# Optimization experiments

Measured on AMD Instinct MI355X. Metric: run time of the kernel, lower is better.

## Reference

```python
import jax, jax.numpy as jnp
import numpy as np

FS = 3          # filter_size
B, C, H, W = 16, 256, 96, 96
BN_EPS = 1e-5


def setup_inputs() -> dict:
    key = jax.random.key(0)
    ks = jax.random.split(key, 6)
    s = 0.05
    return {
        "x": jax.random.normal(ks[0], (B, C, H, W), jnp.float32),
        "convoluted": jax.random.normal(ks[1], (B, C, H, W), jnp.float32),
        # filter_gen_conv: 1x1 Conv2d(C -> C)
        "w_gen": jax.random.normal(ks[2], (C, C, 1, 1), jnp.float32) * s,
        "b_gen": jax.random.normal(ks[3], (C,), jnp.float32) * s,
        # c1: 3x3 Conv2d(C -> C) + BatchNorm2d(C) + ReLU
        "w_c1": jax.random.normal(ks[4], (C, C, 3, 3), jnp.float32) * s,
        "b_c1": jax.random.normal(ks[5], (C,), jnp.float32) * s,
        "gamma": jnp.ones((C,), jnp.float32),
        "beta": jnp.zeros((C,), jnp.float32),
    }


def reference(x, convoluted, w_gen, b_gen, w_c1, b_c1, gamma, beta):
    b, c, h, w = x.shape
    # adaptive_avg_pool2d(x, FS): H,W divisible by FS -> uniform bins
    pooled = x.reshape(b, c, FS, h // FS, FS, w // FS).mean(axis=(3, 5))  # [b,c,FS,FS]
    # 1x1 conv generating per-sample per-channel filters
    gen = jnp.einsum('bcij,oc->boij', pooled, w_gen[:, :, 0, 0]) + b_gen[None, :, None, None]

    # c1: conv3x3 (pad 1) + BatchNorm (training-mode batch stats) + ReLU
    y = jax.lax.conv_general_dilated(
        convoluted, w_c1, window_strides=(1, 1), padding=((1, 1), (1, 1)),
        dimension_numbers=('NCHW', 'OIHW', 'NCHW')) + b_c1[None, :, None, None]
    mu = y.mean(axis=(0, 2, 3), keepdims=True)
    var = y.var(axis=(0, 2, 3), keepdims=True)
    y = (y - mu) * jax.lax.rsqrt(var + BN_EPS)
    y = jax.nn.relu(y * gamma[None, :, None, None] + beta[None, :, None, None])

    # dynamic per-sample depthwise conv: groups = b*c, symmetric pad (FS odd)
    y = y.reshape(1, b * c, h, w)
    filt = gen.reshape(b * c, 1, FS, FS)
    pad = (FS - 1) // 2
    out = jax.lax.conv_general_dilated(
        y, filt, window_strides=(1, 1), padding=((pad, pad), (pad, pad)),
        feature_group_count=b * c, dimension_numbers=('NCHW', 'OIHW', 'NCHW'))
    return out.reshape(b, c, h, w)
```

## Files before the change

kernel.cpp:

```cpp
#include <hip/hip_runtime.h>

typedef __bf16 bf16x8 __attribute__((ext_vector_type(8)));
typedef float f32x4 __attribute__((ext_vector_type(4)));

static __device__ __forceinline__ ushort f2b(float f) {
    uint32_t x = __float_as_uint(f);
    x += 0x7fffu + ((x >> 16) & 1u);
    return (ushort)(x >> 16);
}
static __device__ __forceinline__ float b2f(ushort u) {
    return __uint_as_float(((uint32_t)u) << 16);
}

typedef const __attribute__((address_space(1))) uint32_t gu32;
typedef __attribute__((address_space(3))) uint32_t lu32;
static __device__ __forceinline__ void gl_lds16(const void* g, void* l) {
    __builtin_amdgcn_global_load_lds((gu32*)g, (lu32*)l, 16, 0, 0);
}

__global__ __launch_bounds__(256) void pool_k(const float* __restrict__ x,
                                              float* __restrict__ pooled) {
    const int bc  = blockIdx.x;
    const int tid = threadIdx.x;
    const int lane = tid & 63, wv = tid >> 6;
    const float4* p4 = (const float4*)(x + (size_t)bc * 9216);
    __shared__ float red[4][9];
#pragma unroll
    for (int bi = 0; bi < 3; ++bi) {
#pragma unroll
        for (int bj = 0; bj < 3; ++bj) {
            int row = bi * 32 + (tid >> 3);
            int c4  = bj * 8 + (tid & 7);
            float4 f = p4[row * 24 + c4];
            float s = f.x + f.y + f.z + f.w;
#pragma unroll
            for (int off = 32; off; off >>= 1) s += __shfl_down(s, off);
            if (lane == 0) red[wv][bi * 3 + bj] = s;
        }
    }
    __syncthreads();
    if (tid < 9) {
        float s = red[0][tid] + red[1][tid] + red[2][tid] + red[3][tid];
        pooled[(size_t)bc * 9 + tid] = s * (1.0f / 1024.0f);
    }
}

__global__ __launch_bounds__(256) void gen_k(const float* __restrict__ pooled,
                                             const float* __restrict__ wgen,
                                             const float* __restrict__ bgen,
                                             float* __restrict__ gen) {
    __shared__ float pl[256];
    const int b = blockIdx.x / 9, ij = blockIdx.x % 9;
    const int o = threadIdx.x;
    pl[o] = pooled[((size_t)b * 256 + o) * 9 + ij];
    __syncthreads();
    float a = bgen[o];
    const float4* wg4 = (const float4*)(wgen + (size_t)o * 256);
    const float4* pl4 = (const float4*)pl;
#pragma unroll 4
    for (int q = 0; q < 64; ++q) {
        float4 w = wg4[q], p = pl4[q];
        a += w.x * p.x + w.y * p.y + w.z * p.z + w.w * p.w;
    }
    gen[((size_t)b * 256 + o) * 9 + ij] = a;
}

__global__ __launch_bounds__(256) void wtr_k(const float* __restrict__ wc1,
                                             ushort* __restrict__ wtr) {
    int g = blockIdx.x * 256 + threadIdx.x;
    int step = g >> 10;
    int hi   = (g >> 8) & 3;
    int row  = g & 255;
    int ch = step / 9, tap = step - ch * 9;
    int cbase = ch * 32 + hi * 8;
    ushort tmp[8];
#pragma unroll
    for (int j = 0; j < 8; ++j)
        tmp[j] = f2b(wc1[(size_t)row * 2304 + (size_t)(cbase + j) * 9 + tap]);
    *(uint4*)(wtr + (size_t)g * 8) = *(const uint4*)tmp;
}

__global__ __launch_bounds__(512) void conv_k(const float* __restrict__ xin,
                                              const ushort* __restrict__ wtr,
                                              const float* __restrict__ bc1,
                                              ushort* __restrict__ yb) {
    __shared__ ushort Al[2][8192];
    __shared__ ushort Bl[15680];

    const int blk = blockIdx.x;
    const int b = blk / 48, hg = blk % 48, h0 = hg * 2;
    const int tid = threadIdx.x;
    const int lane = tid & 63, wv = tid >> 6;
    const int wm = wv & 3, wn = wv >> 2;
    const int lo = lane & 15, hi = lane >> 4;

    if (tid < 256) {
        int row = tid >> 6, pxp = ((tid >> 5) & 1) ? 97 : 0, c = tid & 31;
        Bl[(row * 98 + pxp) * 40 + c] = 0;
    }

    const int aoff0 = wv * 1024 + lane * 8;
    const int aoff1 = aoff0 + 512;

    const float* gsrc[6];
    int loff[6];
    bool vld[6];
#pragma unroll
    for (int it = 0; it < 6; ++it) {
        int id = tid + it * 512;
        int c = id & 31, rq = id >> 5;
        int row = rq / 24, q = rq - row * 24;
        int r = h0 + row - 1;
        vld[it] = ((unsigned)r < 96u);
        int rs = vld[it] ? r : 0;
        gsrc[it] = xin + (size_t)b * 2359296 + (size_t)c * 9216 + rs * 96 + q * 4;
        loff[it] = (row * 98 + q * 4 + 1) * 40 + c;
    }

    int aro[4];
#pragma unroll
    for (int mi = 0; mi < 4; ++mi)
        aro[mi] = hi * 2048 + (wm * 64 + mi * 16 + lo) * 8;

    f32x4 acc[4][6] = {};
    float4 f[6];

    gl_lds16(wtr + aoff0, &Al[0][wv * 1024]);
    gl_lds16(wtr + aoff1, &Al[0][wv * 1024 + 512]);
#pragma unroll
    for (int it = 0; it < 6; ++it) f[it] = *(const float4*)gsrc[it];
#pragma unroll
    for (int it = 0; it < 6; ++it) {
        ushort u0 = 0, u1 = 0, u2 = 0, u3 = 0;
        if (vld[it]) { u0 = f2b(f[it].x); u1 = f2b(f[it].y);
                       u2 = f2b(f[it].z); u3 = f2b(f[it].w); }
        ushort* wp = &Bl[loff[it]];
        wp[0] = u0; wp[40] = u1; wp[80] = u2; wp[120] = u3;
    }
    __syncthreads();

    int stp = 0;
    for (int ch = 0; ch < 8; ++ch) {
        if (ch < 7) {
#pragma unroll
            for (int it = 0; it < 6; ++it)
                f[it] = *(const float4*)(gsrc[it] + (size_t)(ch + 1) * 294912);
        }
#pragma unroll
        for (int tap = 0; tap < 9; ++tap, ++stp) {
            const int buf = stp & 1;
            if (stp < 71) {
                const ushort* as = wtr + (size_t)(stp + 1) * 8192;
                gl_lds16(as + aoff0, &Al[buf ^ 1][wv * 1024]);
                gl_lds16(as + aoff1, &Al[buf ^ 1][wv * 1024 + 512]);
            }
            const int dy = tap / 3, dx = tap % 3;
            bf16x8 af[4], bfr[6];
            const ushort* Ab = &Al[buf][0];
#pragma unroll
            for (int mi = 0; mi < 4; ++mi)
                af[mi] = *(const bf16x8*)(Ab + aro[mi]);
            const ushort* Bp = &Bl[((wn + dy) * 98 + lo + dx) * 40 + hi * 8];
#pragma unroll
            for (int ni = 0; ni < 6; ++ni)
                bfr[ni] = *(const bf16x8*)(Bp + ni * 640);
#pragma unroll
            for (int mi = 0; mi < 4; ++mi)
#pragma unroll
                for (int ni = 0; ni < 6; ++ni)
                    acc[mi][ni] = __builtin_amdgcn_mfma_f32_16x16x32_bf16(
                        af[mi], bfr[ni], acc[mi][ni], 0, 0, 0);
            if (tap == 8) {
                if (ch < 7) {
                    __syncthreads();
#pragma unroll
                    for (int it = 0; it < 6; ++it) {
                        ushort u0 = 0, u1 = 0, u2 = 0, u3 = 0;
                        if (vld[it]) { u0 = f2b(f[it].x); u1 = f2b(f[it].y);
                                       u2 = f2b(f[it].z); u3 = f2b(f[it].w); }
                        ushort* wp = &Bl[loff[it]];
                        wp[0] = u0; wp[40] = u1; wp[80] = u2; wp[120] = u3;
                    }
                    __syncthreads();
                }
            } else {
                __syncthreads();
            }
        }
    }

    const size_t ybase = (size_t)b * 2359296 + (size_t)(h0 + wn) * 96;
#pragma unroll
    for (int mi = 0; mi < 4; ++mi) {
        const int o0 = wm * 64 + mi * 16 + hi * 4;
#pragma unroll
        for (int rr = 0; rr < 4; ++rr) {
            const int o = o0 + rr;
            const float bias = bc1[o];
#pragma unroll
            for (int ni = 0; ni < 6; ++ni) {
                const int px = ni * 16 + lo;
                yb[ybase + (size_t)o * 9216 + px] = f2b(acc[mi][ni][rr] + bias);
            }
        }
    }
}

__global__ __launch_bounds__(256) void bnstat_k(const ushort* __restrict__ yb,
                                                float* __restrict__ part) {
    const int bc = blockIdx.x, tid = threadIdx.x;
    const ushort4* p4 = (const ushort4*)(yb + (size_t)bc * 9216);
    float s = 0.f, s2 = 0.f;
#pragma unroll
    for (int it = 0; it < 9; ++it) {
        ushort4 u = p4[tid + it * 256];
        float a = b2f(u.x), bb = b2f(u.y), c = b2f(u.z), d = b2f(u.w);
        s  += a + bb + c + d;
        s2 += a * a + bb * bb + c * c + d * d;
    }
    const int lane = tid & 63, wv = tid >> 6;
#pragma unroll
    for (int off = 32; off; off >>= 1) {
        s += __shfl_down(s, off);
        s2 += __shfl_down(s2, off);
    }
    __shared__ float r1[4], r2[4];
    if (lane == 0) { r1[wv] = s; r2[wv] = s2; }
    __syncthreads();
    if (tid == 0) part[bc]        = r1[0] + r1[1] + r1[2] + r1[3];
    if (tid == 1) part[4096 + bc] = r2[0] + r2[1] + r2[2] + r2[3];
}

__global__ __launch_bounds__(256) void bnfin_k(const float* __restrict__ part,
                                               const float* __restrict__ gamma,
                                               const float* __restrict__ beta,
                                               float* __restrict__ bnp) {
    const int c = threadIdx.x;
    float s = 0.f, s2 = 0.f;
#pragma unroll
    for (int b = 0; b < 16; ++b) {
        s  += part[b * 256 + c];
        s2 += part[4096 + b * 256 + c];
    }
    const float invN = 1.0f / 147456.0f;
    float mu  = s * invN;
    float var = s2 * invN - mu * mu;
    float sc  = gamma[c] * rsqrtf(var + 1e-5f);
    bnp[c]       = sc;
    bnp[256 + c] = beta[c] - mu * sc;
}

__global__ __launch_bounds__(256) void dw_k(const ushort* __restrict__ yb,
                                            const float* __restrict__ gen,
                                            const float* __restrict__ bnp,
                                            float* __restrict__ out) {
    __shared__ float pl[9216];
    const int bc = blockIdx.x, tid = threadIdx.x;
    const int c = bc & 255;
    const float sc = bnp[c], sh = bnp[256 + c];
    const ushort4* p4 = (const ushort4*)(yb + (size_t)bc * 9216);
#pragma unroll
    for (int it = 0; it < 9; ++it) {
        int v = tid + it * 256;
        ushort4 u = p4[v];
        float4 f;
        f.x = fmaxf(b2f(u.x) * sc + sh, 0.f);
        f.y = fmaxf(b2f(u.y) * sc + sh, 0.f);
        f.z = fmaxf(b2f(u.z) * sc + sh, 0.f);
        f.w = fmaxf(b2f(u.w) * sc + sh, 0.f);
        *(float4*)&pl[v * 4] = f;
    }
    float g[9];
    const float* gp = gen + (size_t)bc * 9;
#pragma unroll
    for (int k = 0; k < 9; ++k) g[k] = gp[k];
    __syncthreads();
    float* op = out + (size_t)bc * 9216;
#pragma unroll
    for (int it = 0; it < 36; ++it) {
        int i = tid + it * 256;
        int row = i / 96, col = i - row * 96;
        float a = 0.f;
#pragma unroll
        for (int dy = 0; dy < 3; ++dy) {
            int rr = row + dy - 1;
            if (rr < 0 || rr >= 96) continue;
#pragma unroll
            for (int dxq = 0; dxq < 3; ++dxq) {
                int cc = col + dxq - 1;
                if (cc < 0 || cc >= 96) continue;
                a += pl[rr * 96 + cc] * g[dy * 3 + dxq];
            }
        }
        op[i] = a;
    }
}

extern "C" void kernel_launch(void* const* d_in, const int* in_sizes, int n_in,
                              void* d_out, int out_size, void* d_ws, size_t ws_size,
                              hipStream_t stream) {
    const float* x       = (const float*)d_in[0];
    const float* conv_in = (const float*)d_in[1];
    const float* w_gen   = (const float*)d_in[2];
    const float* b_gen   = (const float*)d_in[3];
    const float* w_c1    = (const float*)d_in[4];
    const float* b_c1    = (const float*)d_in[5];
    const float* gamma   = (const float*)d_in[6];
    const float* beta    = (const float*)d_in[7];
    float* out = (float*)d_out;

    char* ws = (char*)d_ws;
    float*  pooled = (float*)(ws + 0);
    float*  gen    = (float*)(ws + 147456);
    ushort* wtr    = (ushort*)(ws + 294912);
    float*  part   = (float*)(ws + 1474560);
    float*  bnp    = (float*)(ws + 1507328);
    ushort* yb     = (ushort*)(ws + 1509376);

    pool_k  <<<4096, 256, 0, stream>>>(x, pooled);
    gen_k   <<<144,  256, 0, stream>>>(pooled, w_gen, b_gen, gen);
    wtr_k   <<<288,  256, 0, stream>>>(w_c1, wtr);
    conv_k  <<<768,  512, 0, stream>>>(conv_in, wtr, b_c1, yb);
    bnstat_k<<<4096, 256, 0, stream>>>(yb, part);
    bnfin_k <<<1,    256, 0, stream>>>(part, gamma, beta, bnp);
    dw_k    <<<4096, 256, 0, stream>>>(yb, gen, bnp, out);
}
```

Baseline: 383.0 us.

## Fuse BN statistics into conv epilogue and load weights directly to registers

The conv kernel now accumulates per-channel sum and sum-of-squares in its epilogue and writes partials, so the separate bnstat pass that re-read the bf16 conv output is gone. A new per-channel reduction kernel replaces the single-block finalize. Weight tiles now go straight from global memory into registers with double buffering instead of through LDS via global_load_lds. This drops one LDS buffer and many barriers, restructuring the channel-chunk loop into pairs. The cost is more register pressure and global weight loads that are not shared across waves.

```diff
diff --git a/kernel.cpp b/kernel.cpp
--- a/kernel.cpp
+++ b/kernel.cpp
@@ -10,12 +10,6 @@
 }
 static __device__ __forceinline__ float b2f(ushort u) {
     return __uint_as_float(((uint32_t)u) << 16);
-}
-
-typedef const __attribute__((address_space(1))) uint32_t gu32;
-typedef __attribute__((address_space(3))) uint32_t lu32;
-static __device__ __forceinline__ void gl_lds16(const void* g, void* l) {
-    __builtin_amdgcn_global_load_lds((gu32*)g, (lu32*)l, 16, 0, 0);
 }
 
 __global__ __launch_bounds__(256) void pool_k(const float* __restrict__ x,
@@ -69,22 +63,22 @@
                                              ushort* __restrict__ wtr) {
     int g = blockIdx.x * 256 + threadIdx.x;
     int step = g >> 10;
-    int hi   = (g >> 8) & 3;
-    int row  = g & 255;
+    int row  = (g >> 2) & 255;
+    int c8   = g & 3;
     int ch = step / 9, tap = step - ch * 9;
-    int cbase = ch * 32 + hi * 8;
+    int cb = ch * 32 + c8 * 8;
     ushort tmp[8];
 #pragma unroll
     for (int j = 0; j < 8; ++j)
-        tmp[j] = f2b(wc1[(size_t)row * 2304 + (size_t)(cbase + j) * 9 + tap]);
+        tmp[j] = f2b(wc1[(size_t)row * 2304 + (size_t)(cb + j) * 9 + tap]);
     *(uint4*)(wtr + (size_t)g * 8) = *(const uint4*)tmp;
 }
 
 __global__ __launch_bounds__(512) void conv_k(const float* __restrict__ xin,
                                               const ushort* __restrict__ wtr,
                                               const float* __restrict__ bc1,
-                                              ushort* __restrict__ yb) {
-    __shared__ ushort Al[2][8192];
+                                              ushort* __restrict__ yb,
+                                              float* __restrict__ part) {
     __shared__ ushort Bl[15680];
 
     const int blk = blockIdx.x;
@@ -98,9 +92,6 @@
         int row = tid >> 6, pxp = ((tid >> 5) & 1) ? 97 : 0, c = tid & 31;
         Bl[(row * 98 + pxp) * 40 + c] = 0;
     }
-
-    const int aoff0 = wv * 1024 + lane * 8;
-    const int aoff1 = aoff0 + 512;
 
     const float* gsrc[6];
     int loff[6];
@@ -117,74 +108,74 @@
         loff[it] = (row * 98 + q * 4 + 1) * 40 + c;
     }
 
-    int aro[4];
-#pragma unroll
-    for (int mi = 0; mi < 4; ++mi)
-        aro[mi] = hi * 2048 + (wm * 64 + mi * 16 + lo) * 8;
+    float4 f[6];
+    auto stageB = [&]() {
+#pragma unroll
+        for (int it = 0; it < 6; ++it) {
+            ushort u0 = 0, u1 = 0, u2 = 0, u3 = 0;
+            if (vld[it]) { u0 = f2b(f[it].x); u1 = f2b(f[it].y);
+                           u2 = f2b(f[it].z); u3 = f2b(f[it].w); }
+            ushort* wp = &Bl[loff[it]];
+            wp[0] = u0; wp[40] = u1; wp[80] = u2; wp[120] = u3;
+        }
+    };
+
+    const int agrain = (wm * 64 + lo) * 4 + hi;
 
     f32x4 acc[4][6] = {};
-    float4 f[6];
-
-    gl_lds16(wtr + aoff0, &Al[0][wv * 1024]);
-    gl_lds16(wtr + aoff1, &Al[0][wv * 1024 + 512]);
+    uint4 abuf[2][4];
+
+    {
+        const uint4* Ap = (const uint4*)wtr + agrain;
+#pragma unroll
+        for (int mi = 0; mi < 4; ++mi) abuf[0][mi] = Ap[mi * 64];
+    }
 #pragma unroll
     for (int it = 0; it < 6; ++it) f[it] = *(const float4*)gsrc[it];
-#pragma unroll
-    for (int it = 0; it < 6; ++it) {
-        ushort u0 = 0, u1 = 0, u2 = 0, u3 = 0;
-        if (vld[it]) { u0 = f2b(f[it].x); u1 = f2b(f[it].y);
-                       u2 = f2b(f[it].z); u3 = f2b(f[it].w); }
-        ushort* wp = &Bl[loff[it]];
-        wp[0] = u0; wp[40] = u1; wp[80] = u2; wp[120] = u3;
-    }
-    __syncthreads();
-
-    int stp = 0;
-    for (int ch = 0; ch < 8; ++ch) {
-        if (ch < 7) {
-#pragma unroll
-            for (int it = 0; it < 6; ++it)
-                f[it] = *(const float4*)(gsrc[it] + (size_t)(ch + 1) * 294912);
-        }
-#pragma unroll
-        for (int tap = 0; tap < 9; ++tap, ++stp) {
-            const int buf = stp & 1;
-            if (stp < 71) {
-                const ushort* as = wtr + (size_t)(stp + 1) * 8192;
-                gl_lds16(as + aoff0, &Al[buf ^ 1][wv * 1024]);
-                gl_lds16(as + aoff1, &Al[buf ^ 1][wv * 1024 + 512]);
-            }
+    stageB();
+    __syncthreads();
+
+    for (int k = 0; k < 4; ++k) {
+#pragma unroll
+        for (int it = 0; it < 6; ++it)
+            f[it] = *(const float4*)(gsrc[it] + (size_t)(2 * k + 1) * 294912);
+#pragma unroll
+        for (int t = 0; t < 18; ++t) {
+            const int cur = t & 1;
+            if (t < 17 || k < 3) {
+                const uint4* Ap =
+                    (const uint4*)(wtr + (size_t)(k * 18 + t + 1) * 8192) + agrain;
+#pragma unroll
+                for (int mi = 0; mi < 4; ++mi) abuf[cur ^ 1][mi] = Ap[mi * 64];
+            }
+            const int tap = (t < 9) ? t : t - 9;
             const int dy = tap / 3, dx = tap % 3;
-            bf16x8 af[4], bfr[6];
-            const ushort* Ab = &Al[buf][0];
-#pragma unroll
-            for (int mi = 0; mi < 4; ++mi)
-                af[mi] = *(const bf16x8*)(Ab + aro[mi]);
+            bf16x8 bfr[6];
             const ushort* Bp = &Bl[((wn + dy) * 98 + lo + dx) * 40 + hi * 8];
 #pragma unroll
             for (int ni = 0; ni < 6; ++ni)
                 bfr[ni] = *(const bf16x8*)(Bp + ni * 640);
 #pragma unroll
-            for (int mi = 0; mi < 4; ++mi)
+            for (int mi = 0; mi < 4; ++mi) {
+                const bf16x8 af = *(const bf16x8*)&abuf[cur][mi];
 #pragma unroll
                 for (int ni = 0; ni < 6; ++ni)
                     acc[mi][ni] = __builtin_amdgcn_mfma_f32_16x16x32_bf16(
-                        af[mi], bfr[ni], acc[mi][ni], 0, 0, 0);
-            if (tap == 8) {
-                if (ch < 7) {
-                    __syncthreads();
-#pragma unroll
-                    for (int it = 0; it < 6; ++it) {
-                        ushort u0 = 0, u1 = 0, u2 = 0, u3 = 0;
-                        if (vld[it]) { u0 = f2b(f[it].x); u1 = f2b(f[it].y);
-                                       u2 = f2b(f[it].z); u3 = f2b(f[it].w); }
-                        ushort* wp = &Bl[loff[it]];
-                        wp[0] = u0; wp[40] = u1; wp[80] = u2; wp[120] = u3;
-                    }
-                    __syncthreads();
+                        af, bfr[ni], acc[mi][ni], 0, 0, 0);
+            }
+            if (t == 8) {
+                __syncthreads();
+                stageB();
+                __syncthreads();
+                if (k < 3) {
+#pragma unroll
+                    for (int it = 0; it < 6; ++it)
+                        f[it] = *(const float4*)(gsrc[it] + (size_t)(2 * k + 2) * 294912);
                 }
-            } else {
+            } else if (t == 17 && k < 3) {
                 __syncthreads();
+                stageB();
+                __syncthreads();
             }
         }
     }
@@ -192,62 +183,69 @@
     const size_t ybase = (size_t)b * 2359296 + (size_t)(h0 + wn) * 96;
 #pragma unroll
     for (int mi = 0; mi < 4; ++mi) {
-        const int o0 = wm * 64 + mi * 16 + hi * 4;
+        float s[4], s2[4];
 #pragma unroll
         for (int rr = 0; rr < 4; ++rr) {
-            const int o = o0 + rr;
+            const int o = wm * 64 + mi * 16 + hi * 4 + rr;
             const float bias = bc1[o];
+            float sv = 0.f, sv2 = 0.f;
 #pragma unroll
             for (int ni = 0; ni < 6; ++ni) {
                 const int px = ni * 16 + lo;
-                yb[ybase + (size_t)o * 9216 + px] = f2b(acc[mi][ni][rr] + bias);
-            }
-        }
-    }
-}
-
-__global__ __launch_bounds__(256) void bnstat_k(const ushort* __restrict__ yb,
-                                                float* __restrict__ part) {
-    const int bc = blockIdx.x, tid = threadIdx.x;
-    const ushort4* p4 = (const ushort4*)(yb + (size_t)bc * 9216);
-    float s = 0.f, s2 = 0.f;
-#pragma unroll
-    for (int it = 0; it < 9; ++it) {
-        ushort4 u = p4[tid + it * 256];
-        float a = b2f(u.x), bb = b2f(u.y), c = b2f(u.z), d = b2f(u.w);
-        s  += a + bb + c + d;
-        s2 += a * a + bb * bb + c * c + d * d;
-    }
-    const int lane = tid & 63, wv = tid >> 6;
-#pragma unroll
-    for (int off = 32; off; off >>= 1) {
-        s += __shfl_down(s, off);
-        s2 += __shfl_down(s2, off);
-    }
-    __shared__ float r1[4], r2[4];
-    if (lane == 0) { r1[wv] = s; r2[wv] = s2; }
-    __syncthreads();
-    if (tid == 0) part[bc]        = r1[0] + r1[1] + r1[2] + r1[3];
-    if (tid == 1) part[4096 + bc] = r2[0] + r2[1] + r2[2] + r2[3];
-}
-
-__global__ __launch_bounds__(256) void bnfin_k(const float* __restrict__ part,
+                float v = acc[mi][ni][rr] + bias;
+                yb[ybase + (size_t)o * 9216 + px] = f2b(v);
+                sv += v; sv2 += v * v;
+            }
+            s[rr] = sv; s2[rr] = sv2;
+        }
+#pragma unroll
+        for (int off = 1; off < 16; off <<= 1) {
+#pragma unroll
+            for (int rr = 0; rr < 4; ++rr) {
+                s[rr]  += __shfl_xor(s[rr], off);
+                s2[rr] += __shfl_xor(s2[rr], off);
+            }
+        }
+        if (lo == 0) {
+#pragma unroll
+            for (int rr = 0; rr < 4; ++rr) {
+                const int o = wm * 64 + mi * 16 + hi * 4 + rr;
+                part[(size_t)o * 1536 + blk * 2 + wn]          = s[rr];
+                part[393216 + (size_t)o * 1536 + blk * 2 + wn] = s2[rr];
+            }
+        }
+    }
+}
+
+__global__ __launch_bounds__(256) void bnred_k(const float* __restrict__ part,
                                                const float* __restrict__ gamma,
                                                const float* __restrict__ beta,
                                                float* __restrict__ bnp) {
-    const int c = threadIdx.x;
+    const int o = blockIdx.x, t = threadIdx.x;
+    const float* p0 = part + (size_t)o * 1536;
+    const float* p1 = p0 + 393216;
     float s = 0.f, s2 = 0.f;
 #pragma unroll
-    for (int b = 0; b < 16; ++b) {
-        s  += part[b * 256 + c];
-        s2 += part[4096 + b * 256 + c];
-    }
-    const float invN = 1.0f / 147456.0f;
-    float mu  = s * invN;
-    float var = s2 * invN - mu * mu;
-    float sc  = gamma[c] * rsqrtf(var + 1e-5f);
-    bnp[c]       = sc;
-    bnp[256 + c] = beta[c] - mu * sc;
+    for (int k = 0; k < 6; ++k) { s += p0[t + k * 256]; s2 += p1[t + k * 256]; }
+    const int lane = t & 63, wv = t >> 6;
+#pragma unroll
+    for (int off = 32; off; off >>= 1) {
+        s  += __shfl_down(s, off);
+        s2 += __shfl_down(s2, off);
+    }
+    __shared__ float r1[4], r2[4];
+    if (lane == 0) { r1[wv] = s; r2[wv] = s2; }
+    __syncthreads();
+    if (t == 0) {
+        float S  = r1[0] + r1[1] + r1[2] + r1[3];
+        float S2 = r2[0] + r2[1] + r2[2] + r2[3];
+        const float invN = 1.0f / 147456.0f;
+        float mu  = S * invN;
+        float var = S2 * invN - mu * mu;
+        float sc  = gamma[o] * rsqrtf(var + 1e-5f);
+        bnp[o]       = sc;
+        bnp[256 + o] = beta[o] - mu * sc;
+    }
 }
 
 __global__ __launch_bounds__(256) void dw_k(const ushort* __restrict__ yb,
@@ -314,14 +312,13 @@
     float*  gen    = (float*)(ws + 147456);
     ushort* wtr    = (ushort*)(ws + 294912);
     float*  part   = (float*)(ws + 1474560);
-    float*  bnp    = (float*)(ws + 1507328);
-    ushort* yb     = (ushort*)(ws + 1509376);
-
-    pool_k  <<<4096, 256, 0, stream>>>(x, pooled);
-    gen_k   <<<144,  256, 0, stream>>>(pooled, w_gen, b_gen, gen);
-    wtr_k   <<<288,  256, 0, stream>>>(w_c1, wtr);
-    conv_k  <<<768,  512, 0, stream>>>(conv_in, wtr, b_c1, yb);
-    bnstat_k<<<4096, 256, 0, stream>>>(yb, part);
-    bnfin_k <<<1,    256, 0, stream>>>(part, gamma, beta, bnp);
-    dw_k    <<<4096, 256, 0, stream>>>(yb, gen, bnp, out);
-}
+    float*  bnp    = (float*)(ws + 4620288);
+    ushort* yb     = (ushort*)(ws + 4622336);
+
+    pool_k <<<4096, 256, 0, stream>>>(x, pooled);
+    gen_k  <<<144,  256, 0, stream>>>(pooled, w_gen, b_gen, gen);
+    wtr_k  <<<288,  256, 0, stream>>>(w_c1, wtr);
+    conv_k <<<768,  512, 0, stream>>>(conv_in, wtr, b_c1, yb, part);
+    bnred_k<<<256,  256, 0, stream>>>(part, gamma, beta, bnp);
+    dw_k   <<<4096, 256, 0, stream>>>(yb, gen, bnp, out);
+}
```

Measured after the change: 358.2 us. 1.07x faster.
